# Performance work log

Measured on AMD Instinct MI355X. Metric: run time of the kernel, lower is better.

The kernel has to match this reference:

```python
import jax, jax.numpy as jnp
import numpy as np

B, S_SRC, S_TGT, H, V = 32, 128, 64, 300, 32000


def setup_inputs() -> dict:
    key = jax.random.key(0)
    ks = jax.random.split(key, 16)

    def n(k, shape, scale=0.05):
        return jax.random.normal(k, shape, dtype=jnp.float32) * scale

    return {
        "x": jax.random.randint(ks[0], (B, S_SRC), 0, V),
        "y": jax.random.randint(ks[1], (B, S_TGT), 0, V),
        "h0": jax.random.normal(ks[2], (B, H), dtype=jnp.float32),  # encoder initNormState (L=1 squeezed)
        "EN": n(ks[3], (V, H)),
        "ZH": n(ks[4], (V, H)),
        "enc_Wih": n(ks[5], (H, H)),
        "enc_Whh": n(ks[6], (H, H)),
        "enc_bih": n(ks[7], (H,)),
        "enc_bhh": n(ks[8], (H,)),
        "dec_Wih": n(ks[9], (H, H)),
        "dec_Whh": n(ks[10], (H, H)),
        "dec_bih": n(ks[11], (H,)),
        "dec_bhh": n(ks[12], (H,)),
        "W_out": n(ks[13], (V, H)),
        "b_out": n(ks[14], (V,)),
    }


def reference(x, y, h0, EN, ZH, enc_Wih, enc_Whh, enc_bih, enc_bhh,
              dec_Wih, dec_Whh, dec_bih, dec_bhh, W_out, b_out):
    # ---- encoder: 1-layer tanh RNN over source embeddings ----
    xe = EN[x]  # [B, S_src, H]

    def enc_step(h, xt):  # xt: [B, H]
        h = jnp.tanh(xt @ enc_Wih.T + enc_bih + h @ enc_Whh.T + enc_bhh)
        return h, None

    c, _ = jax.lax.scan(enc_step, h0, jnp.swapaxes(xe, 0, 1))  # c: [B, H] final hidden

    # ---- decoder: original loop always feeds encoder state c (never the updated
    # hidden) to the RNNCell; with teacher forcing (start_TF_rate=1.0) every step
    # uses y_in[t], so all T steps vectorize into one batched computation. ----
    ye = ZH[y]  # [B, T, H]
    dec_state_term = c @ dec_Whh.T + dec_bhh  # [B, H], shared across all steps
    h_dec = jnp.tanh(ye @ dec_Wih.T + dec_bih + dec_state_term[:, None, :])  # [B, T, H]
    out = h_dec @ W_out.T + b_out  # [B, T, V]
    return out
```

## Files before the change

### kernel.cpp

```cpp
#include <hip/hip_runtime.h>
#include <hip/hip_bf16.h>
#include <stdint.h>

#define BB 32
#define S_SRC 128
#define S_TGT 64
#define H 300
#define VV 32000
#define M_ROWS (BB * S_TGT)
#define KP 320

#define MEGA_T 640
#define ENC_BLK 32
#define HDEC_BLK 128
#define WCVT_BLK 96

typedef __attribute__((ext_vector_type(8))) __bf16 bf16x8;
typedef __attribute__((ext_vector_type(4))) float f32x4;
typedef __attribute__((ext_vector_type(4))) unsigned short u16x4;
typedef __attribute__((ext_vector_type(2))) __fp16 f16x2;

#if defined(__has_builtin)
#if __has_builtin(__builtin_amdgcn_fdot2)
#define HAVE_FDOT2 1
#endif
#endif

__device__ inline unsigned short f2bf(float f) {
    union { float f; unsigned u; } v; v.f = f;
    unsigned r = (v.u + 0x7FFF + ((v.u >> 16) & 1)) >> 16;
    return (unsigned short)r;
}

__device__ __forceinline__ float ftanh(float x) {
    float e = __builtin_amdgcn_exp2f(x * 2.8853900817779268f);
    return 1.0f - 2.0f * __builtin_amdgcn_rcpf(e + 1.0f);
}

__device__ __forceinline__ float fdot2(f16x2 a, f16x2 b, float c) {
#ifdef HAVE_FDOT2
    return __builtin_amdgcn_fdot2(a, b, c, false);
#else
    return c + (float)a.x * (float)b.x + (float)a.y * (float)b.y;
#endif
}

__device__ __forceinline__ void gl_lds16(const void* g, void* l) {
    __builtin_amdgcn_global_load_lds(
        (const __attribute__((address_space(1))) void*)g,
        (__attribute__((address_space(3))) void*)l, 16, 0, 0);
}

__global__ void transpose2(const float* W0, const float* W1, float* dst) {
    const float* srcs[2] = {W0, W1};
    const float* src = srcs[blockIdx.z];
    float* d = dst + (size_t)blockIdx.z * (H * H);
    __shared__ float tile[32][33];
    int j0 = blockIdx.y * 32, k0 = blockIdx.x * 32;
    for (int r = threadIdx.y; r < 32; r += blockDim.y) {
        int j = j0 + r, k = k0 + threadIdx.x;
        tile[r][threadIdx.x] = (j < H && k < H) ? src[(size_t)j * H + k] : 0.f;
    }
    __syncthreads();
    for (int r = threadIdx.y; r < 32; r += blockDim.y) {
        int k = k0 + r, j = j0 + threadIdx.x;
        if (k < H && j < H) d[(size_t)k * H + j] = tile[threadIdx.x][r];
    }
}

#define RPB 8
__global__ __launch_bounds__(192) void pproj(const int* __restrict__ x,
                                             const float* __restrict__ EN,
                                             const float* __restrict__ WihT,
                                             const float* __restrict__ bih,
                                             const float* __restrict__ bhh,
                                             float* __restrict__ P) {
    __shared__ float xe[RPB][H];
    int m0 = blockIdx.x * RPB;
    int tid = threadIdx.x;
    for (int r = 0; r < RPB; ++r) {
        int idx = x[m0 + r];
        for (int c = tid; c < H; c += 192) xe[r][c] = EN[(size_t)idx * H + c];
    }
    __syncthreads();
    if (tid < 150) {
        int j = tid * 2;
        float a0[RPB], a1[RPB];
#pragma unroll
        for (int r = 0; r < RPB; ++r) { a0[r] = 0.f; a1[r] = 0.f; }
        const float* wp = WihT + j;
        for (int k = 0; k < H; ++k) {
            float2 w = *reinterpret_cast<const float2*>(wp + (size_t)k * H);
#pragma unroll
            for (int r = 0; r < RPB; ++r) {
                float xv = xe[r][k];
                a0[r] += xv * w.x; a1[r] += xv * w.y;
            }
        }
        float b0 = bih[j] + bhh[j], b1 = bih[j + 1] + bhh[j + 1];
#pragma unroll
        for (int r = 0; r < RPB; ++r) {
            P[(size_t)(m0 + r) * H + j]     = a0[r] + b0;
            P[(size_t)(m0 + r) * H + j + 1] = a1[r] + b1;
        }
    }
}

__global__ __launch_bounds__(MEGA_T) void mega(
    const float* __restrict__ h0, const float* __restrict__ P,
    const float* __restrict__ Whh,
    const float* __restrict__ dWhh, const float* __restrict__ dbhh,
    float* __restrict__ s2,
    const int* __restrict__ yv, const float* __restrict__ ZH,
    const float* __restrict__ WihT_d, const float* __restrict__ bih_d,
    float* __restrict__ t1,
    const float* __restrict__ W, unsigned short* __restrict__ Wb) {
    __shared__ union {
        __fp16 hb[2][304];
        float  ye[16][304];
    } L;
    int blk = blockIdx.x, tid = threadIdx.x;

    if (blk < ENC_BLK) {
        int b = blk;
        bool act = tid < 600;
        int j = tid >> 1, half = tid & 1;
        f16x2 w[76];
        if (act) {
            const float* wr = Whh + (size_t)j * H + half * 150;
#pragma unroll
            for (int i = 0; i < 75; ++i) {
                float2 f = *reinterpret_cast<const float2*>(wr + 2 * i);
                w[i] = __builtin_amdgcn_cvt_pkrtz(f.x, f.y);
            }
            w[75] = __builtin_amdgcn_cvt_pkrtz(0.f, 0.f);
        }
        if (act && half == 0) {
            int pos = j < 150 ? j : j + 2;
            L.hb[0][pos] = (__fp16)h0[(size_t)b * H + j];
        }
        if (tid >= 600 && tid < 608) {
            int pi = tid - 600, bufi = pi >> 2, q = pi & 3;
            int idx = (q < 2) ? (150 + q) : (302 + (q - 2));
            L.hb[bufi][idx] = (__fp16)0.f;
        }
        __syncthreads();

        const float* Pb = P + (size_t)b * S_SRC * H;
        int cur = 0;
        for (int t = 0; t < S_SRC; ++t) {
            float pv = 0.f;
            if (act && half == 0) pv = Pb[(size_t)t * H + j];
            if (act) {
                float a0 = 0.f, a1 = 0.f, a2 = 0.f, a3 = 0.f;
                const uint2* hp =
                    reinterpret_cast<const uint2*>(&L.hb[cur][half * 152]);
#pragma unroll
                for (int i = 0; i < 38; i += 2) {
                    uint2 qa = hp[i];
                    uint2 qb = hp[i + 1];
                    a0 = fdot2(w[2 * i],     __builtin_bit_cast(f16x2, qa.x), a0);
                    a1 = fdot2(w[2 * i + 1], __builtin_bit_cast(f16x2, qa.y), a1);
                    a2 = fdot2(w[2 * i + 2], __builtin_bit_cast(f16x2, qb.x), a2);
                    a3 = fdot2(w[2 * i + 3], __builtin_bit_cast(f16x2, qb.y), a3);
                }
                float a = (a0 + a1) + (a2 + a3);
                float tot = a + __shfl_xor(a, 1, 64);
                if (half == 0) {
                    float hv = ftanh(tot + pv);
                    int pos = j < 150 ? j : j + 2;
                    L.hb[cur ^ 1][pos] = (__fp16)hv;
                }
            }
            __syncthreads();
            cur ^= 1;
        }
        if (act) {
            const float* wr = dWhh + (size_t)j * H + half * 150;
            const uint2* hp = reinterpret_cast<const uint2*>(&L.hb[cur][half * 152]);
            float a0 = 0.f, a1 = 0.f;
#pragma unroll
            for (int i = 0; i < 37; ++i) {
                uint2 q = hp[i];
                f16x2 hA = __builtin_bit_cast(f16x2, q.x);
                f16x2 hB = __builtin_bit_cast(f16x2, q.y);
                float4 wf = *reinterpret_cast<const float4*>(wr + 4 * i);
                a0 += wf.x * (float)hA.x + wf.y * (float)hA.y;
                a1 += wf.z * (float)hB.x + wf.w * (float)hB.y;
            }
            {
                f16x2 hA = __builtin_bit_cast(f16x2,
                    reinterpret_cast<const uint*>(&L.hb[cur][half * 152])[74]);
                float2 wf = *reinterpret_cast<const float2*>(wr + 148);
                a0 += wf.x * (float)hA.x + wf.y * (float)hA.y;
            }
            float a = a0 + a1;
            float tot = a + __shfl_xor(a, 1, 64);
            if (half == 0) s2[(size_t)b * H + j] = tot + dbhh[j];
        }
    } else if (blk < ENC_BLK + HDEC_BLK) {
        int bi = blk - ENC_BLK;
        int m0 = bi * 16;
        for (int i = tid; i < 16 * 304; i += MEGA_T) {
            int r = i / 304, cc = i - r * 304;
            L.ye[r][cc] = (cc < H) ? ZH[(size_t)yv[m0 + r] * H + cc] : 0.f;
        }
        __syncthreads();
        if (tid < 600) {
            int rg = tid / 150, jp = tid - rg * 150, j0 = 2 * jp;
            float a[4][2] = {};
            const float* wp = WihT_d + j0;
            for (int k = 0; k < H; k += 2) {
                float2 wa = *reinterpret_cast<const float2*>(wp + (size_t)k * H);
                float2 wb = *reinterpret_cast<const float2*>(wp + (size_t)(k + 1) * H);
#pragma unroll
                for (int r = 0; r < 4; ++r) {
                    float2 x = *reinterpret_cast<const float2*>(&L.ye[rg * 4 + r][k]);
                    a[r][0] += x.x * wa.x + x.y * wb.x;
                    a[r][1] += x.x * wa.y + x.y * wb.y;
                }
            }
            float b0 = bih_d[j0], b1 = bih_d[j0 + 1];
#pragma unroll
            for (int r = 0; r < 4; ++r) {
                *reinterpret_cast<float2*>(&t1[(size_t)(m0 + rg * 4 + r) * 304 + j0]) =
                    make_float2(a[r][0] + b0, a[r][1] + b1);
            }
        }
    } else if (Wb != nullptr) {
        for (int id = (blk - (ENC_BLK + HDEC_BLK)) * MEGA_T + tid; id < VV * 80;
             id += WCVT_BLK * MEGA_T) {
            int row = id / 80, cq = id - row * 80;
            int k = cq * 4;
            u16x4 o;
            if (k < H) {
                float4 f = *reinterpret_cast<const float4*>(W + (size_t)row * H + k);
                o[0] = f2bf(f.x); o[1] = f2bf(f.y); o[2] = f2bf(f.z); o[3] = f2bf(f.w);
            } else {
                o[0] = 0; o[1] = 0; o[2] = 0; o[3] = 0;
            }
            *reinterpret_cast<u16x4*>(Wb + (size_t)row * KP + k) = o;
        }
    }
}

__global__ __launch_bounds__(256) void hdec_fin(const float* __restrict__ t1,
                                                const float* __restrict__ s2,
                                                unsigned short* __restrict__ hdec) {
    int blk = blockIdx.x, tid = threadIdx.x;
    for (int i = tid; i < 8 * KP; i += 256) {
        int r = i / KP, j = i - r * KP;
        int m = blk * 8 + r, b = m >> 6;
        unsigned short v = 0;
        if (j < H)
            v = f2bf(ftanh(t1[(size_t)m * 304 + j] + s2[(size_t)b * H + j]));
        hdec[(size_t)m * KP + j] = v;
    }
}

__global__ __launch_bounds__(512, 2) void gemm3(const unsigned short* __restrict__ A,
                                                const unsigned short* __restrict__ Wb,
                                                const float* __restrict__ bout,
                                                float* __restrict__ out) {
    __shared__ unsigned short Al[2][256 * 64];
    __shared__ unsigned short Bl[2][256 * 64];
    int tid = threadIdx.x;
    int lane = tid & 63, wv = tid >> 6;
    int wm = wv >> 2, wn = wv & 3;

    int orig = blockIdx.x;
    int wg = (orig & 7) * 125 + (orig >> 3);
    int mi = wg & 7, ni = wg >> 3;
    int m0 = mi * 256, n0 = ni * 256;

    int rowb = tid >> 3;
    int sc = (tid & 7) ^ (rowb & 7);

    f32x4 acc[8][4];
    f32x4 zero = {0.f, 0.f, 0.f, 0.f};
#pragma unroll
    for (int i = 0; i < 8; ++i)
#pragma unroll
        for (int j = 0; j < 4; ++j) acc[i][j] = zero;

#pragma unroll
    for (int i = 0; i < 4; ++i) {
        int row = i * 64 + rowb;
        gl_lds16(A + (size_t)(m0 + row) * KP + sc * 8, &Al[0][(i * 512 + tid) * 8]);
    }
#pragma unroll
    for (int i = 0; i < 4; ++i) {
        int row = i * 64 + rowb;
        gl_lds16(Wb + (size_t)(n0 + row) * KP + sc * 8, &Bl[0][(i * 512 + tid) * 8]);
    }

    for (int t = 0; t < 5; ++t) {
        __syncthreads();
        int buf = t & 1;
        if (t < 4) {
            int k0 = (t + 1) * 64, nb = buf ^ 1;
#pragma unroll
            for (int i = 0; i < 4; ++i) {
                int row = i * 64 + rowb;
                gl_lds16(A + (size_t)(m0 + row) * KP + k0 + sc * 8,
                         &Al[nb][(i * 512 + tid) * 8]);
            }
#pragma unroll
            for (int i = 0; i < 4; ++i) {
                int row = i * 64 + rowb;
                gl_lds16(Wb + (size_t)(n0 + row) * KP + k0 + sc * 8,
                         &Bl[nb][(i * 512 + tid) * 8]);
            }
        }
#pragma unroll
        for (int ks = 0; ks < 2; ++ks) {
            bf16x8 af[8], bb[4];
            int slot = (ks * 4 + (lane >> 4)) ^ (lane & 7);
#pragma unroll
            for (int i = 0; i < 8; ++i) {
                int row = wm * 128 + i * 16 + (lane & 15);
                af[i] = *reinterpret_cast<const bf16x8*>(&Al[buf][row * 64 + slot * 8]);
            }
#pragma unroll
            for (int j = 0; j < 4; ++j) {
                int row = wn * 64 + j * 16 + (lane & 15);
                bb[j] = *reinterpret_cast<const bf16x8*>(&Bl[buf][row * 64 + slot * 8]);
            }
#pragma unroll
            for (int i = 0; i < 8; ++i)
#pragma unroll
                for (int j = 0; j < 4; ++j)
                    acc[i][j] = __builtin_amdgcn_mfma_f32_16x16x32_bf16(
                        af[i], bb[j], acc[i][j], 0, 0, 0);
        }
    }

#pragma unroll
    for (int j = 0; j < 4; ++j) {
        int col = n0 + wn * 64 + j * 16 + (lane & 15);
        float bo = bout[col];
#pragma unroll
        for (int i = 0; i < 8; ++i) {
            int rb = m0 + wm * 128 + i * 16 + (lane >> 4) * 4;
            f32x4 v = acc[i][j];
#pragma unroll
            for (int r = 0; r < 4; ++r)
                out[(size_t)(rb + r) * VV + col] = v[r] + bo;
        }
    }
}

#define LDSW 40
__global__ __launch_bounds__(256) void gemm_out(const unsigned short* __restrict__ A,
                                                const float* __restrict__ W,
                                                const float* __restrict__ bout,
                                                float* __restrict__ out) {
    __shared__ __align__(16) unsigned short Alds[128 * LDSW];
    __shared__ __align__(16) unsigned short Bl[128 * LDSW];
    int tid = threadIdx.x;
    int lane = tid & 63, wv = tid >> 6;
    int wm = wv >> 1, wn = wv & 1;
    int m0 = blockIdx.y * 128, n0 = blockIdx.x * 128;

    f32x4 acc[4][4];
    f32x4 zero = {0.f, 0.f, 0.f, 0.f};
#pragma unroll
    for (int i = 0; i < 4; ++i)
#pragma unroll
        for (int jj = 0; jj < 4; ++jj) acc[i][jj] = zero;

    for (int k0 = 0; k0 < KP; k0 += 32) {
#pragma unroll
        for (int s = 0; s < 2; ++s) {
            int slot = tid + s * 256;
            int row = slot >> 2, c16 = slot & 3;
            uint4 v = *reinterpret_cast<const uint4*>(
                &A[(size_t)(m0 + row) * KP + k0 + c16 * 8]);
            *reinterpret_cast<uint4*>(&Alds[row * LDSW + c16 * 8]) = v;
        }
#pragma unroll
        for (int s = 0; s < 2; ++s) {
            int slot = tid + s * 256;
            int row = slot >> 2, c8 = slot & 3;
            int k = k0 + c8 * 8;
            __align__(16) unsigned short tmp[8];
            if (k + 7 < H) {
                const float* src = &W[(size_t)(n0 + row) * H + k];
                float4 f0 = *reinterpret_cast<const float4*>(src);
                float4 f1 = *reinterpret_cast<const float4*>(src + 4);
                tmp[0] = f2bf(f0.x); tmp[1] = f2bf(f0.y);
                tmp[2] = f2bf(f0.z); tmp[3] = f2bf(f0.w);
                tmp[4] = f2bf(f1.x); tmp[5] = f2bf(f1.y);
                tmp[6] = f2bf(f1.z); tmp[7] = f2bf(f1.w);
            } else {
#pragma unroll
                for (int jv = 0; jv < 8; ++jv) {
                    int kk = k + jv;
                    tmp[jv] = (kk < H) ? f2bf(W[(size_t)(n0 + row) * H + kk])
                                       : (unsigned short)0;
                }
            }
            *reinterpret_cast<uint4*>(&Bl[row * LDSW + c8 * 8]) =
                *reinterpret_cast<const uint4*>(tmp);
        }
        __syncthreads();
        bf16x8 af[4], bfm[4];
#pragma unroll
        for (int i = 0; i < 4; ++i) {
            int row = wm * 64 + i * 16 + (lane & 15);
            af[i] = *reinterpret_cast<const bf16x8*>(&Alds[row * LDSW + (lane >> 4) * 8]);
        }
#pragma unroll
        for (int i = 0; i < 4; ++i) {
            int row = wn * 64 + i * 16 + (lane & 15);
            bfm[i] = *reinterpret_cast<const bf16x8*>(&Bl[row * LDSW + (lane >> 4) * 8]);
        }
#pragma unroll
        for (int i = 0; i < 4; ++i)
#pragma unroll
            for (int jj = 0; jj < 4; ++jj)
                acc[i][jj] = __builtin_amdgcn_mfma_f32_16x16x32_bf16(
                    af[i], bfm[jj], acc[i][jj], 0, 0, 0);
        __syncthreads();
    }
#pragma unroll
    for (int jj = 0; jj < 4; ++jj) {
        int col = n0 + wn * 64 + jj * 16 + (lane & 15);
        float bo = bout[col];
#pragma unroll
        for (int i = 0; i < 4; ++i) {
            int rb = m0 + wm * 64 + i * 16 + (lane >> 4) * 4;
            f32x4 v = acc[i][jj];
#pragma unroll
            for (int r = 0; r < 4; ++r)
                out[(size_t)(rb + r) * VV + col] = v[r] + bo;
        }
    }
}

extern "C" void kernel_launch(void* const* d_in, const int* in_sizes, int n_in,
                              void* d_out, int out_size, void* d_ws, size_t ws_size,
                              hipStream_t stream) {
    const int*   x       = (const int*)d_in[0];
    const int*   y       = (const int*)d_in[1];
    const float* h0      = (const float*)d_in[2];
    const float* EN      = (const float*)d_in[3];
    const float* ZH      = (const float*)d_in[4];
    const float* enc_Wih = (const float*)d_in[5];
    const float* enc_Whh = (const float*)d_in[6];
    const float* enc_bih = (const float*)d_in[7];
    const float* enc_bhh = (const float*)d_in[8];
    const float* dec_Wih = (const float*)d_in[9];
    const float* dec_Whh = (const float*)d_in[10];
    const float* dec_bih = (const float*)d_in[11];
    const float* dec_bhh = (const float*)d_in[12];
    const float* W_out   = (const float*)d_in[13];
    const float* b_out   = (const float*)d_in[14];
    float* out = (float*)d_out;
    char* base = (char*)d_ws;

    const size_t needA = 22549120, needB = 2069120;
    bool bigws = (ws_size >= needA);
    if (!bigws && ws_size < needB) return;

    float* WT = (float*)base;
    float *s2_;
    unsigned short *hdec, *Wb = nullptr;
    if (bigws) {
        Wb   = (unsigned short*)(base + 720000);
        s2_  = (float*)(base + 21200000);
        hdec = (unsigned short*)(base + 21238400);
    } else {
        s2_  = (float*)(base + 720000);
        hdec = (unsigned short*)(base + 758400);
    }
    float* P  = out;
    float* t1 = out + 2000000;

    transpose2<<<dim3(10, 10, 2), dim3(32, 8), 0, stream>>>(enc_Wih, dec_Wih, WT);
    pproj<<<(BB * S_SRC) / RPB, 192, 0, stream>>>(x, EN, WT, enc_bih, enc_bhh, P);
    int mega_grid = bigws ? (ENC_BLK + HDEC_BLK + WCVT_BLK) : (ENC_BLK + HDEC_BLK);
    mega<<<mega_grid, MEGA_T, 0, stream>>>(h0, P, enc_Whh, dec_Whh, dec_bhh, s2_,
                                           y, ZH, WT + 90000, dec_bih, t1,
                                           W_out, Wb);
    hdec_fin<<<M_ROWS / 8, 256, 0, stream>>>(t1, s2_, hdec);
    if (bigws) {
        gemm3<<<1000, 512, 0, stream>>>(hdec, Wb, b_out, out);
    } else {
        gemm_out<<<dim3(VV / 128, M_ROWS / 128), 256, 0, stream>>>(hdec, W_out, b_out, out);
    }
}
```

Measured before the change: 264.6 us.

## Replace output GEMM with 128x128-tile, 4-stage pipelined kernel

The output projection GEMM moves from 256x256 tiles with 512 threads and a double buffer over K=64 steps to 128x128 tiles with 256 threads and a 4-buffer ring over K=32 steps. Loads are issued three stages ahead and waited on with explicit vmcnt counts, so a single barrier per step replaces the full sync, and MFMA issue is raised with setprio. Smaller tiles give 4000 workgroups, which should spread work and tail more evenly across CUs. The cost is more redundant A/B global traffic and more loop iterations per tile.

```diff
diff --git a/kernel.cpp b/kernel.cpp
--- a/kernel.cpp
+++ b/kernel.cpp
@@ -258,90 +258,93 @@
     }
 }
 
-__global__ __launch_bounds__(512, 2) void gemm3(const unsigned short* __restrict__ A,
+#define NBUF 4
+__global__ __launch_bounds__(256, 2) void gemm4(const unsigned short* __restrict__ A,
                                                 const unsigned short* __restrict__ Wb,
                                                 const float* __restrict__ bout,
                                                 float* __restrict__ out) {
-    __shared__ unsigned short Al[2][256 * 64];
-    __shared__ unsigned short Bl[2][256 * 64];
+    __shared__ unsigned short Al[NBUF][128 * 32];
+    __shared__ unsigned short Bl[NBUF][128 * 32];
     int tid = threadIdx.x;
     int lane = tid & 63, wv = tid >> 6;
-    int wm = wv >> 2, wn = wv & 3;
+    int wm = wv >> 1, wn = wv & 1;
 
     int orig = blockIdx.x;
-    int wg = (orig & 7) * 125 + (orig >> 3);
-    int mi = wg & 7, ni = wg >> 3;
-    int m0 = mi * 256, n0 = ni * 256;
-
-    int rowb = tid >> 3;
-    int sc = (tid & 7) ^ (rowb & 7);
-
-    f32x4 acc[8][4];
+    int wg = (orig & 7) * 500 + (orig >> 3);
+    int mi = wg & 15, ni = wg >> 4;
+    int m0 = mi * 128, n0 = ni * 128;
+
+    int rowq = tid >> 2;
+    int scn = (tid & 3) ^ (rowq & 3);
+
+    const unsigned short* Ab = A + (size_t)m0 * KP;
+    const unsigned short* Bb = Wb + (size_t)n0 * KP;
+
+    f32x4 acc[4][4];
     f32x4 zero = {0.f, 0.f, 0.f, 0.f};
 #pragma unroll
-    for (int i = 0; i < 8; ++i)
+    for (int i = 0; i < 4; ++i)
 #pragma unroll
         for (int j = 0; j < 4; ++j) acc[i][j] = zero;
 
-#pragma unroll
-    for (int i = 0; i < 4; ++i) {
-        int row = i * 64 + rowb;
-        gl_lds16(A + (size_t)(m0 + row) * KP + sc * 8, &Al[0][(i * 512 + tid) * 8]);
-    }
-#pragma unroll
-    for (int i = 0; i < 4; ++i) {
-        int row = i * 64 + rowb;
-        gl_lds16(Wb + (size_t)(n0 + row) * KP + sc * 8, &Bl[0][(i * 512 + tid) * 8]);
-    }
-
-    for (int t = 0; t < 5; ++t) {
-        __syncthreads();
-        int buf = t & 1;
-        if (t < 4) {
-            int k0 = (t + 1) * 64, nb = buf ^ 1;
-#pragma unroll
-            for (int i = 0; i < 4; ++i) {
-                int row = i * 64 + rowb;
-                gl_lds16(A + (size_t)(m0 + row) * KP + k0 + sc * 8,
-                         &Al[nb][(i * 512 + tid) * 8]);
-            }
-#pragma unroll
-            for (int i = 0; i < 4; ++i) {
-                int row = i * 64 + rowb;
-                gl_lds16(Wb + (size_t)(n0 + row) * KP + k0 + sc * 8,
-                         &Bl[nb][(i * 512 + tid) * 8]);
-            }
-        }
-#pragma unroll
-        for (int ks = 0; ks < 2; ++ks) {
-            bf16x8 af[8], bb[4];
-            int slot = (ks * 4 + (lane >> 4)) ^ (lane & 7);
-#pragma unroll
-            for (int i = 0; i < 8; ++i) {
-                int row = wm * 128 + i * 16 + (lane & 15);
-                af[i] = *reinterpret_cast<const bf16x8*>(&Al[buf][row * 64 + slot * 8]);
-            }
-#pragma unroll
-            for (int j = 0; j < 4; ++j) {
-                int row = wn * 64 + j * 16 + (lane & 15);
-                bb[j] = *reinterpret_cast<const bf16x8*>(&Bl[buf][row * 64 + slot * 8]);
-            }
-#pragma unroll
-            for (int i = 0; i < 8; ++i)
-#pragma unroll
-                for (int j = 0; j < 4; ++j)
-                    acc[i][j] = __builtin_amdgcn_mfma_f32_16x16x32_bf16(
-                        af[i], bb[j], acc[i][j], 0, 0, 0);
-        }
-    }
+#define STAGE(T)                                                               \
+    {                                                                          \
+        int kk_ = (T) * 32;                                                    \
+        int bf_ = (T) & 3;                                                     \
+        _Pragma("unroll")                                                      \
+        for (int s_ = 0; s_ < 2; ++s_) {                                       \
+            int row_ = s_ * 64 + rowq;                                         \
+            gl_lds16(Ab + (size_t)row_ * KP + kk_ + scn * 8,                   \
+                     &Al[bf_][(s_ * 256 + tid) * 8]);                          \
+        }                                                                      \
+        _Pragma("unroll")                                                      \
+        for (int s_ = 0; s_ < 2; ++s_) {                                       \
+            int row_ = s_ * 64 + rowq;                                         \
+            gl_lds16(Bb + (size_t)row_ * KP + kk_ + scn * 8,                   \
+                     &Bl[bf_][(s_ * 256 + tid) * 8]);                          \
+        }                                                                      \
+    }
+
+    STAGE(0) STAGE(1) STAGE(2)
+
+#pragma unroll
+    for (int t = 0; t < 10; ++t) {
+        __builtin_amdgcn_sched_barrier(0);
+        if (t < 8)       asm volatile("s_waitcnt vmcnt(8)" ::: "memory");
+        else if (t == 8) asm volatile("s_waitcnt vmcnt(4)" ::: "memory");
+        else             asm volatile("s_waitcnt vmcnt(0)" ::: "memory");
+        __builtin_amdgcn_s_barrier();
+        __builtin_amdgcn_sched_barrier(0);
+        if (t + 3 < 10) STAGE(t + 3)
+        int bf = t & 3;
+        bf16x8 af[4], bb[4];
+#pragma unroll
+        for (int i = 0; i < 4; ++i) {
+            int rowA = wm * 64 + i * 16 + (lane & 15);
+            int chA = (lane >> 4) ^ (rowA & 3);
+            af[i] = *reinterpret_cast<const bf16x8*>(&Al[bf][rowA * 32 + chA * 8]);
+            int rowB = wn * 64 + i * 16 + (lane & 15);
+            int chB = (lane >> 4) ^ (rowB & 3);
+            bb[i] = *reinterpret_cast<const bf16x8*>(&Bl[bf][rowB * 32 + chB * 8]);
+        }
+        __builtin_amdgcn_s_setprio(1);
+#pragma unroll
+        for (int i = 0; i < 4; ++i)
+#pragma unroll
+            for (int j = 0; j < 4; ++j)
+                acc[i][j] = __builtin_amdgcn_mfma_f32_16x16x32_bf16(
+                    af[i], bb[j], acc[i][j], 0, 0, 0);
+        __builtin_amdgcn_s_setprio(0);
+    }
+#undef STAGE
 
 #pragma unroll
     for (int j = 0; j < 4; ++j) {
         int col = n0 + wn * 64 + j * 16 + (lane & 15);
         float bo = bout[col];
 #pragma unroll
-        for (int i = 0; i < 8; ++i) {
-            int rb = m0 + wm * 128 + i * 16 + (lane >> 4) * 4;
+        for (int i = 0; i < 4; ++i) {
+            int rb = m0 + wm * 64 + i * 16 + (lane >> 4) * 4;
             f32x4 v = acc[i][j];
 #pragma unroll
             for (int r = 0; r < 4; ++r)
@@ -485,7 +488,7 @@
                                            W_out, Wb);
     hdec_fin<<<M_ROWS / 8, 256, 0, stream>>>(t1, s2_, hdec);
     if (bigws) {
-        gemm3<<<1000, 512, 0, stream>>>(hdec, Wb, b_out, out);
+        gemm4<<<4000, 256, 0, stream>>>(hdec, Wb, b_out, out);
     } else {
         gemm_out<<<dim3(VV / 128, M_ROWS / 128), 256, 0, stream>>>(hdec, W_out, b_out, out);
     }
```

Result: no change. 263.5 us (-0.4%).
